# Kernel tuning notes

Measured on AMD Instinct MI355X. Metric: run time of the kernel, lower is better.

Reference implementation:

```python
import jax, jax.numpy as jnp
import numpy as np

HIDDEN = 2048
N_HEADS = 16
HEAD_DIM = 128
N_EXPERTS = 8
TOP_K = 2
INTER = 1024
EPS = 1e-5
ROPE_THETA = 10000.0
T = 2048


def rms_norm(x, w, eps=EPS):
    xf = x.astype(jnp.float32)
    return (xf * jax.lax.rsqrt(jnp.mean(xf * xf, axis=-1, keepdims=True) + eps)).astype(x.dtype) * w


def apply_rope(x, positions):
    # x: [T, H, D], NeoX-style half rotation
    d = x.shape[-1]
    inv_freq = 1.0 / (ROPE_THETA ** (jnp.arange(0, d, 2, dtype=jnp.float32) / d))
    ang = positions.astype(jnp.float32)[:, None] * inv_freq  # [T, D/2]
    cos = jnp.cos(ang)[:, None, :]
    sin = jnp.sin(ang)[:, None, :]
    x1, x2 = jnp.split(x, 2, axis=-1)
    return jnp.concatenate([x1 * cos - x2 * sin, x2 * cos + x1 * sin], axis=-1)


def setup_inputs() -> dict:
    key = jax.random.key(0)
    ks = jax.random.split(key, 8)
    s = 0.02
    return {
        "positions": jnp.arange(T, dtype=jnp.int32),
        "hidden_states": jax.random.normal(ks[0], (T, HIDDEN), jnp.float32),
        "qkv_w": jax.random.normal(ks[1], (3 * HIDDEN, HIDDEN), jnp.float32) * s,
        "o_w": jax.random.normal(ks[2], (HIDDEN, HIDDEN), jnp.float32) * s,
        "q_norm_w": jnp.ones((N_HEADS * HEAD_DIM,), jnp.float32),
        "k_norm_w": jnp.ones((N_HEADS * HEAD_DIM,), jnp.float32),
        "post_attn_norm_w": jnp.ones((HIDDEN,), jnp.float32),
        "post_ffn_norm_w": jnp.ones((HIDDEN,), jnp.float32),
        "gate_w": jax.random.normal(ks[3], (N_EXPERTS, HIDDEN), jnp.float32) * s,
        "w_gate": jax.random.normal(ks[4], (N_EXPERTS, INTER, HIDDEN), jnp.float32) * s,
        "w_up": jax.random.normal(ks[5], (N_EXPERTS, INTER, HIDDEN), jnp.float32) * s,
        "w_down": jax.random.normal(ks[6], (N_EXPERTS, HIDDEN, INTER), jnp.float32) * s,
    }


def attention(positions, x, qkv_w, o_w, q_norm_w, k_norm_w):
    qkv = x @ qkv_w.T  # [T, 3*HIDDEN]
    q, k, v = jnp.split(qkv, 3, axis=-1)
    q = rms_norm(q, q_norm_w)  # norm over full flat q dim (FlexOlmo/OLMoE style)
    k = rms_norm(k, k_norm_w)
    q = apply_rope(q.reshape(T, N_HEADS, HEAD_DIM), positions)
    k = apply_rope(k.reshape(T, N_HEADS, HEAD_DIM), positions)
    v = v.reshape(T, N_HEADS, HEAD_DIM)
    scale = 1.0 / np.sqrt(HEAD_DIM)
    scores = jnp.einsum('thd,shd->hts', q, k) * scale
    mask = jnp.tril(jnp.ones((T, T), bool))
    scores = jnp.where(mask[None], scores, -jnp.inf)
    p = jax.nn.softmax(scores, axis=-1)
    out = jnp.einsum('hts,shd->thd', p, v).reshape(T, HIDDEN)
    return out @ o_w.T


def moe(x, gate_w, w_gate, w_up, w_down):
    logits = (x @ gate_w.T).astype(jnp.float32)  # router_logits.float()
    probs = jax.nn.softmax(logits, axis=-1)
    topv, topi = jax.lax.top_k(probs, TOP_K)  # renormalize=False -> use raw softmax weights
    # dense per-expert combine weights: [T, E]
    wdense = jnp.zeros((T, N_EXPERTS), jnp.float32)
    wdense = jnp.sum(jax.nn.one_hot(topi, N_EXPERTS, dtype=jnp.float32) * topv[..., None], axis=1)
    # detach().clone() before dispatch (inference semantics: value unchanged)
    xe = jax.lax.stop_gradient(x)
    g = jnp.einsum('td,efd->tef', xe, w_gate)
    u = jnp.einsum('td,efd->tef', xe, w_up)
    h = jax.nn.silu(g) * u
    y = jnp.einsum('tef,edf->ted', h, w_down)
    return jnp.einsum('ted,te->td', y, wdense)


def reference(positions, hidden_states, qkv_w, o_w, q_norm_w, k_norm_w,
              post_attn_norm_w, post_ffn_norm_w, gate_w, w_gate, w_up, w_down):
    residual = hidden_states
    h = attention(positions, hidden_states, qkv_w, o_w, q_norm_w, k_norm_w)
    h = rms_norm(h, post_attn_norm_w)
    h = h + residual
    residual = h
    h = moe(h, gate_w, w_gate, w_up, w_down)
    h = rms_norm(h, post_ffn_norm_w)
    return residual + h
```

## Files before the change

kernel.cpp:

```cpp
#include <hip/hip_runtime.h>
#include <hip/hip_bf16.h>
#include <cmath>

#define TT 2048
#define HID 2048
#define NHEADS 16
#define HDIM 128
#define NEXP 8
#define INTERD 1024
#define EPSV 1e-5f

typedef short bf16x8 __attribute__((ext_vector_type(8)));
typedef float f32x4 __attribute__((ext_vector_type(4)));

__device__ __forceinline__ unsigned short f2bf(float f) {
    unsigned int u = __builtin_bit_cast(unsigned int, f);
    unsigned int r = (u + 0x7FFFu + ((u >> 16) & 1u)) >> 16;
    return (unsigned short)r;
}
__device__ __forceinline__ float bf2f(unsigned short h) {
    return __builtin_bit_cast(float, (unsigned int)h << 16);
}

__device__ __forceinline__ void gll16(const void* g, void* l) {
    __builtin_amdgcn_global_load_lds((const __attribute__((address_space(1))) void*)g,
                                     (__attribute__((address_space(3))) void*)l, 16, 0, 0);
}

__device__ __forceinline__ float block_reduce_sum_256(float v, float* red) {
    const int tid = threadIdx.x;
    red[tid] = v;
    __syncthreads();
    for (int s = 128; s > 0; s >>= 1) {
        if (tid < s) red[tid] += red[tid + s];
        __syncthreads();
    }
    float r = red[0];
    __syncthreads();
    return r;
}

__global__ __launch_bounds__(256) void split_f32k(const float* __restrict__ x,
                                                  unsigned short* __restrict__ hi,
                                                  unsigned short* __restrict__ lo, int n4) {
    int i = blockIdx.x * 256 + threadIdx.x;
    if (i >= n4) return;
    float4 v = reinterpret_cast<const float4*>(x)[i];
    float xs[4] = {v.x, v.y, v.z, v.w};
    unsigned short hs[4], ls[4];
#pragma unroll
    for (int u = 0; u < 4; ++u) {
        hs[u] = f2bf(xs[u]);
        ls[u] = f2bf(xs[u] - bf2f(hs[u]));
    }
    uint2 hp; hp.x = hs[0] | ((unsigned)hs[1] << 16); hp.y = hs[2] | ((unsigned)hs[3] << 16);
    uint2 lp; lp.x = ls[0] | ((unsigned)ls[1] << 16); lp.y = ls[2] | ((unsigned)ls[3] << 16);
    *reinterpret_cast<uint2*>(hi + (size_t)i * 4) = hp;
    *reinterpret_cast<uint2*>(lo + (size_t)i * 4) = lp;
}

#define GSTAGE(BUF, K0)                                                             \
    {                                                                               \
        char* base_ = (char*)Smem + (BUF) * 32768;                                  \
        _Pragma("unroll")                                                           \
        for (int i_ = 0; i_ < 2; ++i_) {                                            \
            int c_ = tid + i_ * 256;                                                \
            int r_ = c_ >> 2, s_ = c_ & 3;                                          \
            int ko_ = (K0) + (((s_ ^ ((r_ >> 1) & 3)) & 3) << 3);                   \
            gll16(Ah + (size_t)(m0 + r_) * lda + ko_, base_ + c_ * 16);             \
            gll16(Al + (size_t)(m0 + r_) * lda + ko_, base_ + 8192 + c_ * 16);      \
            gll16(Bh + (size_t)(n0 + r_) * K + ko_, base_ + 16384 + c_ * 16);       \
            gll16(Bl + (size_t)(n0 + r_) * K + ko_, base_ + 24576 + c_ * 16);       \
        }                                                                           \
    }

__global__ __launch_bounds__(256) void gemm_sp(const unsigned short* __restrict__ Ah,
                                               const unsigned short* __restrict__ Al,
                                               const unsigned short* __restrict__ Bh,
                                               const unsigned short* __restrict__ Bl,
                                               float* __restrict__ C, int N, int K, int lda) {
    const int nbx = gridDim.x;
    const int nwg = nbx * gridDim.y;
    const int orig = blockIdx.y * nbx + blockIdx.x;
    const int qq = nwg >> 3, rr = nwg & 7;
    const int xcd = orig & 7, loc = orig >> 3;
    const int wgid = (xcd < rr ? xcd * (qq + 1) : rr * (qq + 1) + (xcd - rr) * qq) + loc;
    const int m0 = (wgid / nbx) * 128, n0 = (wgid % nbx) * 128;

    __shared__ __align__(16) unsigned short Smem[2 * 4 * 128 * 32];
    const int tid = threadIdx.x;
    const int w = tid >> 6, l = tid & 63;
    const int lr = l & 15, lg = l >> 4;
    const int wm = w >> 1, wn = w & 1;

    f32x4 acc[4][4];
#pragma unroll
    for (int i = 0; i < 4; ++i)
#pragma unroll
        for (int j = 0; j < 4; ++j) acc[i][j] = f32x4{0.f, 0.f, 0.f, 0.f};

    const int nks = K >> 5;
    GSTAGE(0, 0);
    int cur = 0;
    for (int ks = 0; ks < nks; ++ks) {
        if (ks + 1 < nks) {
            GSTAGE(cur ^ 1, (ks + 1) << 5);
            asm volatile("s_waitcnt vmcnt(8)" ::: "memory");
        } else {
            asm volatile("s_waitcnt vmcnt(0)" ::: "memory");
        }
        __builtin_amdgcn_s_barrier();
        __builtin_amdgcn_sched_barrier(0);
        char* bb = (char*)Smem + cur * 32768;
        bf16x8 bhf[4], blf[4];
#pragma unroll
        for (int nt = 0; nt < 4; ++nt) {
            int row = wn * 64 + nt * 16 + lr;
            int off = row * 64 + (((lg ^ ((row >> 1) & 3)) & 3) << 4);
            bhf[nt] = *reinterpret_cast<const bf16x8*>(bb + 16384 + off);
            blf[nt] = *reinterpret_cast<const bf16x8*>(bb + 24576 + off);
        }
        __builtin_amdgcn_s_setprio(1);
#pragma unroll
        for (int mt = 0; mt < 4; ++mt) {
            int row = wm * 64 + mt * 16 + lr;
            int off = row * 64 + (((lg ^ ((row >> 1) & 3)) & 3) << 4);
            bf16x8 ahf = *reinterpret_cast<const bf16x8*>(bb + off);
            bf16x8 alf = *reinterpret_cast<const bf16x8*>(bb + 8192 + off);
#pragma unroll
            for (int nt = 0; nt < 4; ++nt) {
                acc[mt][nt] = __builtin_amdgcn_mfma_f32_16x16x32_bf16(ahf, bhf[nt], acc[mt][nt], 0, 0, 0);
                acc[mt][nt] = __builtin_amdgcn_mfma_f32_16x16x32_bf16(ahf, blf[nt], acc[mt][nt], 0, 0, 0);
                acc[mt][nt] = __builtin_amdgcn_mfma_f32_16x16x32_bf16(alf, bhf[nt], acc[mt][nt], 0, 0, 0);
            }
        }
        __builtin_amdgcn_s_setprio(0);
        asm volatile("s_waitcnt lgkmcnt(0)" ::: "memory");
        __builtin_amdgcn_s_barrier();
        __builtin_amdgcn_sched_barrier(0);
        cur ^= 1;
    }
#pragma unroll
    for (int mt = 0; mt < 4; ++mt) {
#pragma unroll
        for (int r = 0; r < 4; ++r) {
            size_t crow = (size_t)(m0 + wm * 64 + mt * 16 + lg * 4 + r) * N;
#pragma unroll
            for (int nt = 0; nt < 4; ++nt)
                C[crow + n0 + wn * 64 + nt * 16 + lr] = acc[mt][nt][r];
        }
    }
}

template<int ABF, int MODE>
__global__ __launch_bounds__(256) void gemm_moe(const void* __restrict__ Ap,
                                                const float* __restrict__ B,
                                                void* __restrict__ Cout,
                                                const float* __restrict__ gsrc,
                                                int N, int K, int lda,
                                                size_t strideB,
                                                const int* __restrict__ gather,
                                                const int* __restrict__ offs,
                                                const int* __restrict__ counts) {
    const int e = blockIdx.z;
    const int cnt = counts[e];
    const int base = offs[e];
    const int m0 = blockIdx.y * 64;
    if (m0 >= cnt) return;
    const int n0 = blockIdx.x * 128;
    const float* Bp = B + (size_t)e * strideB;

    __shared__ unsigned short smA[64 * 64];
    __shared__ unsigned short smB[128 * 64];
    __shared__ int rowsA[64];
    const int tid = threadIdx.x;
    if (tid < 64) {
        int rr = min(m0 + tid, cnt - 1);
        rowsA[tid] = gather ? gather[base + rr] : (base + rr);
    }
    __syncthreads();

    const int w = tid >> 6, l = tid & 63;
    const int lr = l & 15, lg = l >> 4;
    const int wm = w >> 1, wn = w & 1;
    char* sA = (char*)smA;
    char* sB = (char*)smB;

    f32x4 acc[2][4];
#pragma unroll
    for (int i = 0; i < 2; ++i)
#pragma unroll
        for (int j = 0; j < 4; ++j) acc[i][j] = f32x4{0.f, 0.f, 0.f, 0.f};

    for (int k0 = 0; k0 < K; k0 += 64) {
        if (ABF) {
            const unsigned short* Abf = (const unsigned short*)Ap;
#pragma unroll
            for (int i = 0; i < 2; ++i) {
                int slot = tid + i * 256;
                int r = slot >> 3, sg = slot & 7;
                uint4 v = *reinterpret_cast<const uint4*>(&Abf[(size_t)rowsA[r] * lda + k0 + sg * 8]);
                *reinterpret_cast<uint4*>(sA + r * 128 + ((sg * 16) ^ ((r & 7) << 4))) = v;
            }
        } else {
            const float* Af = (const float*)Ap;
#pragma unroll
            for (int i = 0; i < 4; ++i) {
                int slot = tid + i * 256;
                int r = slot >> 4, kq = slot & 15;
                float4 av = *reinterpret_cast<const float4*>(&Af[(size_t)rowsA[r] * lda + k0 + kq * 4]);
                uint2 pk;
                pk.x = (unsigned)f2bf(av.x) | ((unsigned)f2bf(av.y) << 16);
                pk.y = (unsigned)f2bf(av.z) | ((unsigned)f2bf(av.w) << 16);
                *reinterpret_cast<uint2*>(sA + r * 128 + ((kq * 8) ^ ((r & 7) << 4))) = pk;
            }
        }
#pragma unroll
        for (int i = 0; i < 8; ++i) {
            int slot = tid + i * 256;
            int r = slot >> 4, kq = slot & 15;
            float4 bv = *reinterpret_cast<const float4*>(&Bp[(size_t)(n0 + r) * K + k0 + kq * 4]);
            uint2 pk;
            pk.x = (unsigned)f2bf(bv.x) | ((unsigned)f2bf(bv.y) << 16);
            pk.y = (unsigned)f2bf(bv.z) | ((unsigned)f2bf(bv.w) << 16);
            *reinterpret_cast<uint2*>(sB + r * 128 + ((kq * 8) ^ ((r & 7) << 4))) = pk;
        }
        __syncthreads();
#pragma unroll
        for (int kk = 0; kk < 2; ++kk) {
            bf16x8 af[2], bfr[4];
#pragma unroll
            for (int mt = 0; mt < 2; ++mt) {
                int row = wm * 32 + mt * 16 + lr;
                af[mt] = *reinterpret_cast<const bf16x8*>(sA + row * 128 + ((kk * 64 + lg * 16) ^ ((row & 7) << 4)));
            }
#pragma unroll
            for (int nt = 0; nt < 4; ++nt) {
                int row = wn * 64 + nt * 16 + lr;
                bfr[nt] = *reinterpret_cast<const bf16x8*>(sB + row * 128 + ((kk * 64 + lg * 16) ^ ((row & 7) << 4)));
            }
            __builtin_amdgcn_s_setprio(1);
#pragma unroll
            for (int mt = 0; mt < 2; ++mt)
#pragma unroll
                for (int nt = 0; nt < 4; ++nt)
                    acc[mt][nt] = __builtin_amdgcn_mfma_f32_16x16x32_bf16(af[mt], bfr[nt], acc[mt][nt], 0, 0, 0);
            __builtin_amdgcn_s_setprio(0);
        }
        __syncthreads();
    }
#pragma unroll
    for (int mt = 0; mt < 2; ++mt) {
#pragma unroll
        for (int r = 0; r < 4; ++r) {
            int rowl = wm * 32 + mt * 16 + lg * 4 + r;
            if (m0 + rowl < cnt) {
                size_t crow = (size_t)(base + m0 + rowl) * N;
#pragma unroll
                for (int nt = 0; nt < 4; ++nt) {
                    size_t idx = crow + n0 + wn * 64 + nt * 16 + lr;
                    if (MODE == 1) {
                        float g = gsrc[idx];
                        ((unsigned short*)Cout)[idx] = f2bf(g / (1.f + expf(-g)) * acc[mt][nt][r]);
                    } else {
                        ((float*)Cout)[idx] = acc[mt][nt][r];
                    }
                }
            }
        }
    }
}

__global__ __launch_bounds__(256) void qknorm_rope_split(float* __restrict__ qkv,
                                                         const float* __restrict__ qw,
                                                         const float* __restrict__ kw,
                                                         const int* __restrict__ pos) {
    __shared__ float xbuf[2048];
    __shared__ float red[256];
    const int t = blockIdx.x, tid = threadIdx.x;
    unsigned short* row16 = (unsigned short*)(qkv + (size_t)t * 6144);
    const float pf = (float)pos[t];
    float vreg[8];
    const float* vsrc = qkv + (size_t)t * 6144 + 4096;
#pragma unroll
    for (int i = 0; i < 8; ++i) vreg[i] = vsrc[tid + i * 256];
    __syncthreads();
#pragma unroll
    for (int i = 0; i < 8; ++i) {
        int d = tid + i * 256;
        unsigned short hi = f2bf(vreg[i]);
        row16[8192 + d] = hi;
        row16[10240 + d] = f2bf(vreg[i] - bf2f(hi));
    }
    for (int part = 0; part < 2; ++part) {
        const float* x = qkv + (size_t)t * 6144 + part * 2048;
        const float* wn = part ? kw : qw;
        const int sbase = part ? 4096 : 0;
        const float outscale = part ? 1.0f : 0.08838834764831845f;
        float s = 0.f;
#pragma unroll
        for (int i = 0; i < 8; ++i) {
            int d = tid + i * 256;
            float v = x[d];
            xbuf[d] = v;
            s = fmaf(v, v, s);
        }
        float tot = block_reduce_sum_256(s, red);
        float scale = rsqrtf(tot * (1.f / HID) + EPSV);
#pragma unroll
        for (int p = tid; p < 1024; p += 256) {
            int hh = p >> 6, j = p & 63;
            int i1 = hh * 128 + j, i2 = i1 + 64;
            float x1 = xbuf[i1] * scale * wn[i1];
            float x2 = xbuf[i2] * scale * wn[i2];
            float invf = expf(-(float)j * 0.14391156831212787f);
            float ang = pf * invf;
            float sn, cs;
            sincosf(ang, &sn, &cs);
            float o1 = (x1 * cs - x2 * sn) * outscale;
            float o2 = (x2 * cs + x1 * sn) * outscale;
            unsigned short h1_ = f2bf(o1);
            row16[sbase + i1] = h1_;
            row16[sbase + 2048 + i1] = f2bf(o1 - bf2f(h1_));
            unsigned short h2_ = f2bf(o2);
            row16[sbase + i2] = h2_;
            row16[sbase + 2048 + i2] = f2bf(o2 - bf2f(h2_));
        }
        __syncthreads();
    }
}

__global__ __launch_bounds__(256) void kvprep(const unsigned short* __restrict__ qkv16,
                                              unsigned short* __restrict__ kt,
                                              unsigned short* __restrict__ vt) {
    const int C = blockIdx.x;
    const int h = blockIdx.y;
    const int tid = threadIdx.x;
#pragma unroll
    for (int p = 0; p < 2; ++p) {
#pragma unroll
        for (int i = 0; i < 4; ++i) {
            int slot = tid + i * 256;
            int r = slot >> 4, sg = slot & 15;
            uint4 v = *reinterpret_cast<const uint4*>(
                qkv16 + (size_t)(C * 64 + r) * 12288 + 4096 + p * 2048 + h * 128 + (sg ^ (r & 7)) * 8);
            *reinterpret_cast<uint4*>(kt + (size_t)(h * 32 + C) * 16384 + p * 8192 + slot * 8) = v;
        }
    }
    __shared__ unsigned short tile[64 * 128];
    char* tb = (char*)tile;
    for (int p = 0; p < 2; ++p) {
#pragma unroll
        for (int i = 0; i < 4; ++i) {
            int c = tid + i * 256;
            int r = c >> 4, dseg = c & 15;
            uint4 v = *reinterpret_cast<const uint4*>(
                qkv16 + (size_t)(C * 64 + r) * 12288 + 8192 + p * 2048 + h * 128 + dseg * 8);
            int swz = dseg ^ (r & 7) ^ (r >> 3);
            *reinterpret_cast<uint4*>(tb + r * 256 + swz * 16) = v;
        }
        __syncthreads();
        unsigned short* ob = vt + (size_t)(h * 32 + C) * 16384 + p * 8192;
#pragma unroll
        for (int i = 0; i < 4; ++i) {
            int c = tid + i * 256;
            int d = c >> 3, j = c & 7;
            unsigned short tmp[8];
#pragma unroll
            for (int u = 0; u < 8; ++u) {
                int s = 8 * j + u;
                int swz = (d >> 3) ^ (s & 7) ^ (s >> 3);
                tmp[u] = *reinterpret_cast<const unsigned short*>(tb + s * 256 + swz * 16 + (d & 7) * 2);
            }
            *reinterpret_cast<uint4*>(ob + (size_t)d * 64 + ((j ^ (d & 7)) * 8)) =
                *reinterpret_cast<const uint4*>(tmp);
        }
        __syncthreads();
    }
}

#define STAGE1(CIDX)                                                                   \
    {                                                                                  \
        const unsigned short* kb_ = kt + (size_t)(h * 32 + (CIDX)) * 16384;            \
        const unsigned short* vb_ = vt + (size_t)(h * 32 + (CIDX)) * 16384;            \
        _Pragma("unroll")                                                              \
        for (int p_ = 0; p_ < 2; ++p_) {                                               \
            _Pragma("unroll")                                                          \
            for (int i_ = 0; i_ < 4; ++i_) {                                           \
                int slot_ = tid + i_ * 256;                                            \
                gll16(kb_ + p_ * 8192 + slot_ * 8, kvb + p_ * 16384 + slot_ * 16);     \
                gll16(vb_ + p_ * 8192 + slot_ * 8, kvb + 32768 + p_ * 16384 + slot_ * 16); \
            }                                                                          \
        }                                                                              \
    }

__global__ __launch_bounds__(256) void attn_mfma(const unsigned short* __restrict__ qkv16,
                                                 const unsigned short* __restrict__ kt,
                                                 const unsigned short* __restrict__ vt,
                                                 unsigned short* __restrict__ oh,
                                                 unsigned short* __restrict__ ol) {
    const int g = blockIdx.x;
    const int rank = (g < 256) ? g : 767 - g;
    const int h = rank & 15;
    const int t0 = (31 - (rank >> 4)) * 64;
    const int tid = threadIdx.x;
    const int w = tid >> 6, l = tid & 63;
    const int lr = l & 15, lg = l >> 4;
    const size_t RS = 12288;
    __shared__ __align__(16) unsigned short KVs[32768];
    __shared__ unsigned short Ps[4][2 * 16 * 64];
    char* kvb = (char*)KVs;
    char* PsB = (char*)(Ps[w]);

    bf16x8 qh[4], ql[4];
    {
        const unsigned short* qp = qkv16 + (size_t)(t0 + w * 16 + lr) * RS + h * 128 + lg * 8;
#pragma unroll
        for (int kk = 0; kk < 4; ++kk) {
            qh[kk] = *reinterpret_cast<const bf16x8*>(qp + kk * 32);
            ql[kk] = *reinterpret_cast<const bf16x8*>(qp + 2048 + kk * 32);
        }
    }
    f32x4 oacc[8];
#pragma unroll
    for (int dt = 0; dt < 8; ++dt) oacc[dt] = f32x4{0.f, 0.f, 0.f, 0.f};
    float mrun[4] = {-INFINITY, -INFINITY, -INFINITY, -INFINITY};
    float lrun[4] = {0.f, 0.f, 0.f, 0.f};

    for (int s0 = 0; s0 <= t0; s0 += 64) {
        STAGE1(s0 >> 6);
        __syncthreads();
        char* KsB = kvb;
        char* VtB = kvb + 32768;

        f32x4 sc[4];
#pragma unroll
        for (int nt = 0; nt < 4; ++nt) sc[nt] = f32x4{0.f, 0.f, 0.f, 0.f};
        __builtin_amdgcn_s_setprio(1);
#pragma unroll
        for (int kk = 0; kk < 4; ++kk) {
#pragma unroll
            for (int nt = 0; nt < 4; ++nt) {
                int row = nt * 16 + lr;
                int off = row * 256 + ((kk * 64 + lg * 16) ^ ((row & 7) << 4));
                bf16x8 kh = *reinterpret_cast<const bf16x8*>(KsB + off);
                bf16x8 kl = *reinterpret_cast<const bf16x8*>(KsB + 16384 + off);
                sc[nt] = __builtin_amdgcn_mfma_f32_16x16x32_bf16(qh[kk], kh, sc[nt], 0, 0, 0);
                sc[nt] = __builtin_amdgcn_mfma_f32_16x16x32_bf16(ql[kk], kh, sc[nt], 0, 0, 0);
                sc[nt] = __builtin_amdgcn_mfma_f32_16x16x32_bf16(qh[kk], kl, sc[nt], 0, 0, 0);
            }
        }
        __builtin_amdgcn_s_setprio(0);
        float mnew[4], alpha[4], psum[4];
#pragma unroll
        for (int r = 0; r < 4; ++r) {
            int row_t = t0 + w * 16 + lg * 4 + r;
            float mx = mrun[r];
#pragma unroll
            for (int nt = 0; nt < 4; ++nt) {
                int col = s0 + nt * 16 + lr;
                float v = sc[nt][r];
                if (col > row_t) v = -INFINITY;
                sc[nt][r] = v;
                mx = fmaxf(mx, v);
            }
#pragma unroll
            for (int o = 1; o < 16; o <<= 1) mx = fmaxf(mx, __shfl_xor(mx, o));
            mnew[r] = mx;
            alpha[r] = expf(mrun[r] - mx);
            mrun[r] = mx;
            psum[r] = 0.f;
        }
#pragma unroll
        for (int nt = 0; nt < 4; ++nt) {
#pragma unroll
            for (int r = 0; r < 4; ++r) {
                float p = expf(sc[nt][r] - mnew[r]);
                psum[r] += p;
                int prow = lg * 4 + r;
                int off = prow * 128 + (((nt * 16 + lr) * 2) ^ ((prow & 7) << 4));
                unsigned short ph = f2bf(p);
                *reinterpret_cast<unsigned short*>(PsB + off) = ph;
                *reinterpret_cast<unsigned short*>(PsB + 2048 + off) = f2bf(p - bf2f(ph));
            }
        }
#pragma unroll
        for (int r = 0; r < 4; ++r) {
            float s = psum[r];
#pragma unroll
            for (int o = 1; o < 16; o <<= 1) s += __shfl_xor(s, o);
            lrun[r] = lrun[r] * alpha[r] + s;
        }
#pragma unroll
        for (int dt = 0; dt < 8; ++dt)
#pragma unroll
            for (int r = 0; r < 4; ++r) oacc[dt][r] *= alpha[r];
        bf16x8 ph[2], pl[2];
#pragma unroll
        for (int kk = 0; kk < 2; ++kk) {
            int off = lr * 128 + ((kk * 64 + lg * 16) ^ ((lr & 7) << 4));
            ph[kk] = *reinterpret_cast<const bf16x8*>(PsB + off);
            pl[kk] = *reinterpret_cast<const bf16x8*>(PsB + 2048 + off);
        }
        __builtin_amdgcn_s_setprio(1);
#pragma unroll
        for (int dt = 0; dt < 8; ++dt) {
            int row = dt * 16 + lr;
#pragma unroll
            for (int kk = 0; kk < 2; ++kk) {
                int off = row * 128 + ((kk * 64 + lg * 16) ^ ((row & 7) << 4));
                bf16x8 vh = *reinterpret_cast<const bf16x8*>(VtB + off);
                bf16x8 vl = *reinterpret_cast<const bf16x8*>(VtB + 16384 + off);
                oacc[dt] = __builtin_amdgcn_mfma_f32_16x16x32_bf16(ph[kk], vh, oacc[dt], 0, 0, 0);
                oacc[dt] = __builtin_amdgcn_mfma_f32_16x16x32_bf16(ph[kk], vl, oacc[dt], 0, 0, 0);
                oacc[dt] = __builtin_amdgcn_mfma_f32_16x16x32_bf16(pl[kk], vh, oacc[dt], 0, 0, 0);
            }
        }
        __builtin_amdgcn_s_setprio(0);
        __syncthreads();
    }
#pragma unroll
    for (int r = 0; r < 4; ++r) {
        float inv = 1.f / lrun[r];
        int row_t = t0 + w * 16 + lg * 4 + r;
#pragma unroll
        for (int dt = 0; dt < 8; ++dt) {
            float o = oacc[dt][r] * inv;
            unsigned short hb = f2bf(o);
            size_t idx = (size_t)row_t * 2048 + h * 128 + dt * 16 + lr;
            oh[idx] = hb;
            ol[idx] = f2bf(o - bf2f(hb));
        }
    }
}

__global__ __launch_bounds__(256) void add_rmsnorm(const float* __restrict__ resid,
                                                   const float* __restrict__ x,
                                                   const float* __restrict__ w,
                                                   float* __restrict__ out,
                                                   unsigned short* __restrict__ outbf) {
    __shared__ float red[256];
    const int t = blockIdx.x, tid = threadIdx.x;
    const float* xr = x + (size_t)t * HID;
    float v[8];
    float s = 0.f;
#pragma unroll
    for (int i = 0; i < 8; ++i) { v[i] = xr[tid + i * 256]; s = fmaf(v[i], v[i], s); }
    float tot = block_reduce_sum_256(s, red);
    float scale = rsqrtf(tot * (1.f / HID) + EPSV);
#pragma unroll
    for (int i = 0; i < 8; ++i) {
        int d = tid + i * 256;
        float o = resid[(size_t)t * HID + d] + v[i] * scale * w[d];
        out[(size_t)t * HID + d] = o;
        outbf[(size_t)t * HID + d] = f2bf(o);
    }
}

__global__ __launch_bounds__(64) void router_kernel(const float* __restrict__ h1,
                                                    const float* __restrict__ gate_w,
                                                    int* __restrict__ topi, float* __restrict__ topv,
                                                    int* __restrict__ slot_tk, int* __restrict__ counts) {
    const int t = blockIdx.x, lane = threadIdx.x;
    float acc[NEXP] = {};
    const float* x = h1 + (size_t)t * HID;
    for (int d = lane; d < HID; d += 64) {
        float xv = x[d];
#pragma unroll
        for (int e = 0; e < NEXP; ++e) acc[e] = fmaf(xv, gate_w[e * HID + d], acc[e]);
    }
#pragma unroll
    for (int e = 0; e < NEXP; ++e)
#pragma unroll
        for (int off = 32; off > 0; off >>= 1) acc[e] += __shfl_down(acc[e], off);
    if (lane == 0) {
        float mx = acc[0];
        for (int e = 1; e < NEXP; ++e) mx = fmaxf(mx, acc[e]);
        float p[NEXP], se = 0.f;
        for (int e = 0; e < NEXP; ++e) { p[e] = expf(acc[e] - mx); se += p[e]; }
        float inv = 1.f / se;
        for (int e = 0; e < NEXP; ++e) p[e] *= inv;
        int e1 = 0;
        for (int e = 1; e < NEXP; ++e) if (p[e] > p[e1]) e1 = e;
        int e2 = (e1 == 0) ? 1 : 0;
        for (int e = 0; e < NEXP; ++e) if (e != e1 && p[e] > p[e2]) e2 = e;
        topi[t * 2] = e1;     topv[t * 2] = p[e1];
        topi[t * 2 + 1] = e2; topv[t * 2 + 1] = p[e2];
        slot_tk[t * 2]     = atomicAdd(&counts[e1], 1);
        slot_tk[t * 2 + 1] = atomicAdd(&counts[e2], 1);
    }
}

__global__ void scan_kernel(const int* __restrict__ counts, int* __restrict__ offs) {
    int o = 0;
    for (int e = 0; e < NEXP; ++e) { offs[e] = o; o += counts[e]; }
}

__global__ __launch_bounds__(256) void map_kernel(const int* __restrict__ topi,
                                                  const int* __restrict__ slot_tk,
                                                  const int* __restrict__ offs,
                                                  int* __restrict__ token_of_row,
                                                  int* __restrict__ row_of_tk) {
    int idx = blockIdx.x * 256 + threadIdx.x;
    if (idx >= TT * 2) return;
    int e = topi[idx];
    int row = offs[e] + slot_tk[idx];
    token_of_row[row] = idx >> 1;
    row_of_tk[idx] = row;
}

__global__ __launch_bounds__(256) void final_combine(const float* __restrict__ h1,
                                                     const float* __restrict__ ypart,
                                                     const float* __restrict__ topv,
                                                     const int* __restrict__ row_of_tk,
                                                     const float* __restrict__ wffn,
                                                     float* __restrict__ out) {
    __shared__ float red[256];
    const int t = blockIdx.x, tid = threadIdx.x;
    const int r0 = row_of_tk[t * 2], r1 = row_of_tk[t * 2 + 1];
    const float w0 = topv[t * 2], w1 = topv[t * 2 + 1];
    const float* y0 = ypart + (size_t)r0 * HID;
    const float* y1 = ypart + (size_t)r1 * HID;
    float v[8];
    float s = 0.f;
#pragma unroll
    for (int i = 0; i < 8; ++i) {
        int d = tid + i * 256;
        v[i] = w0 * y0[d] + w1 * y1[d];
        s = fmaf(v[i], v[i], s);
    }
    float tot = block_reduce_sum_256(s, red);
    float scale = rsqrtf(tot * (1.f / HID) + EPSV);
#pragma unroll
    for (int i = 0; i < 8; ++i) {
        int d = tid + i * 256;
        out[(size_t)t * HID + d] = h1[(size_t)t * HID + d] + v[i] * scale * wffn[d];
    }
}

extern "C" void kernel_launch(void* const* d_in, const int* in_sizes, int n_in,
                              void* d_out, int out_size, void* d_ws, size_t ws_size,
                              hipStream_t stream) {
    const int*   positions = (const int*)d_in[0];
    const float* hidden    = (const float*)d_in[1];
    const float* qkv_w     = (const float*)d_in[2];
    const float* o_w       = (const float*)d_in[3];
    const float* q_norm_w  = (const float*)d_in[4];
    const float* k_norm_w  = (const float*)d_in[5];
    const float* post_attn = (const float*)d_in[6];
    const float* post_ffn  = (const float*)d_in[7];
    const float* gate_w    = (const float*)d_in[8];
    const float* w_gate    = (const float*)d_in[9];
    const float* w_up      = (const float*)d_in[10];
    const float* w_down    = (const float*)d_in[11];
    float* out = (float*)d_out;

    char* ws = (char*)d_ws;
    size_t off = 0;
    auto alloc = [&](size_t bytes) -> void* {
        void* p = ws + off;
        off += (bytes + 255) & ~(size_t)255;
        return p;
    };
    float*          qkvbuf = (float*)alloc((size_t)TT * 6144 * 4);
    unsigned short* hidsp  = (unsigned short*)alloc((size_t)TT * HID * 2 * 2);
    unsigned short* wsp    = (unsigned short*)alloc(((size_t)6144 * HID * 2 + (size_t)HID * HID * 2) * 2);
    float*          h1     = (float*)alloc((size_t)TT * HID * 4);
    unsigned short* h1bf   = (unsigned short*)alloc((size_t)TT * HID * 2);
    int*   topi   = (int*)alloc(TT * 2 * 4);
    float* topv   = (float*)alloc(TT * 2 * 4);
    int*   slot   = (int*)alloc(TT * 2 * 4);
    int*   rowtk  = (int*)alloc(TT * 2 * 4);
    int*   tokrow = (int*)alloc(TT * 2 * 4);
    int*   counts = (int*)alloc(8 * 4);
    int*   offsb  = (int*)alloc(8 * 4);
    if (off > ws_size) return;

    unsigned short* hid_hi   = hidsp;
    unsigned short* hid_lo   = hidsp + (size_t)TT * HID;
    unsigned short* attnO_hi = hid_hi;
    unsigned short* attnO_lo = hid_lo;
    unsigned short* qkvw_hi = wsp;
    unsigned short* qkvw_lo = wsp + (size_t)6144 * HID;
    unsigned short* ow_hi   = wsp + (size_t)2 * 6144 * HID;
    unsigned short* ow_lo   = ow_hi + (size_t)HID * HID;
    unsigned short* vtbuf   = wsp;
    unsigned short* ktbuf   = wsp + (size_t)TT * HID * 2;
    unsigned short* hinter = (unsigned short*)qkvbuf;
    float*          gbuf   = qkvbuf + (size_t)4096 * INTERD;
    float*          oOut   = qkvbuf + (size_t)8192 * INTERD;
    float*          ypart  = oOut;

    hipMemsetAsync(counts, 0, 8 * sizeof(int), stream);

    dim3 b256(256);
    split_f32k<<<dim3(TT * HID / 4 / 256), b256, 0, stream>>>(hidden, hid_hi, hid_lo, TT * HID / 4);
    split_f32k<<<dim3(6144 * HID / 4 / 256), b256, 0, stream>>>(qkv_w, qkvw_hi, qkvw_lo, 6144 * HID / 4);
    split_f32k<<<dim3(HID * HID / 4 / 256), b256, 0, stream>>>(o_w, ow_hi, ow_lo, HID * HID / 4);
    gemm_sp<<<dim3(6144 / 128, TT / 128), b256, 0, stream>>>(hid_hi, hid_lo, qkvw_hi, qkvw_lo,
                                                             qkvbuf, 6144, HID, HID);
    qknorm_rope_split<<<dim3(TT), b256, 0, stream>>>(qkvbuf, q_norm_w, k_norm_w, positions);
    kvprep<<<dim3(32, NHEADS), b256, 0, stream>>>((const unsigned short*)qkvbuf, ktbuf, vtbuf);
    attn_mfma<<<dim3(512), b256, 0, stream>>>((const unsigned short*)qkvbuf, ktbuf, vtbuf,
                                              attnO_hi, attnO_lo);
    gemm_sp<<<dim3(HID / 128, TT / 128), b256, 0, stream>>>(attnO_hi, attnO_lo, ow_hi, ow_lo,
                                                            oOut, HID, HID, HID);
    add_rmsnorm<<<dim3(TT), b256, 0, stream>>>(hidden, oOut, post_attn, h1, h1bf);
    router_kernel<<<dim3(TT), dim3(64), 0, stream>>>(h1, gate_w, topi, topv, slot, counts);
    scan_kernel<<<1, 1, 0, stream>>>(counts, offsb);
    map_kernel<<<dim3((TT * 2 + 255) / 256), b256, 0, stream>>>(topi, slot, offsb, tokrow, rowtk);
    gemm_moe<1, 0><<<dim3(INTERD / 128, TT * 2 / 64, NEXP), b256, 0, stream>>>(
        h1bf, w_gate, gbuf, nullptr, INTERD, HID, HID, (size_t)INTERD * HID, tokrow, offsb, counts);
    gemm_moe<1, 1><<<dim3(INTERD / 128, TT * 2 / 64, NEXP), b256, 0, stream>>>(
        h1bf, w_up, hinter, gbuf, INTERD, HID, HID, (size_t)INTERD * HID, tokrow, offsb, counts);
    gemm_moe<1, 0><<<dim3(HID / 128, TT * 2 / 64, NEXP), b256, 0, stream>>>(
        hinter, w_down, ypart, nullptr, HID, INTERD, INTERD, (size_t)HID * INTERD, nullptr, offsb, counts);
    final_combine<<<dim3(TT), b256, 0, stream>>>(h1, ypart, topv, rowtk, post_ffn, out);
}
```

Measured before the change: 660.2 us.

## Merge split kernels, drop scan kernel, use LDS-direct A loads, store bf16 MoE output

Merges the three fp32-to-bf16 hi/lo split launches into one kernel and removes the single-thread scan kernel by having each consumer compute expert offsets inline from counts. The MoE GEMM now loads A tiles straight into LDS with global_load_lds, using per-thread row indices computed up front in place of a shared row table and an extra barrier. The down projection writes its partial outputs as bf16 rather than fp32, which halves that write and the final combine's read but adds rounding before the weighted sum. The goal is fewer launches and less memory traffic, at some precision cost.

```diff
diff --git a/kernel.cpp b/kernel.cpp
--- a/kernel.cpp
+++ b/kernel.cpp
@@ -40,11 +40,17 @@
     return r;
 }
 
-__global__ __launch_bounds__(256) void split_f32k(const float* __restrict__ x,
-                                                  unsigned short* __restrict__ hi,
-                                                  unsigned short* __restrict__ lo, int n4) {
-    int i = blockIdx.x * 256 + threadIdx.x;
-    if (i >= n4) return;
+__global__ __launch_bounds__(256) void split3(const float* __restrict__ xh, unsigned short* __restrict__ hh,
+                                              unsigned short* __restrict__ hl,
+                                              const float* __restrict__ xq, unsigned short* __restrict__ qh,
+                                              unsigned short* __restrict__ ql,
+                                              const float* __restrict__ xo, unsigned short* __restrict__ oh,
+                                              unsigned short* __restrict__ ol) {
+    int b = blockIdx.x;
+    const float* x; unsigned short* hi; unsigned short* lo; int i;
+    if (b < 4096)       { x = xh; hi = hh; lo = hl; i = b * 256 + threadIdx.x; }
+    else if (b < 16384) { x = xq; hi = qh; lo = ql; i = (b - 4096) * 256 + threadIdx.x; }
+    else                { x = xo; hi = oh; lo = ol; i = (b - 16384) * 256 + threadIdx.x; }
     float4 v = reinterpret_cast<const float4*>(x)[i];
     float xs[4] = {v.x, v.y, v.z, v.w};
     unsigned short hs[4], ls[4];
@@ -152,40 +158,48 @@
     }
 }
 
-template<int ABF, int MODE>
-__global__ __launch_bounds__(256) void gemm_moe(const void* __restrict__ Ap,
+template<int GATHER, int MODE>
+__global__ __launch_bounds__(256) void gemm_moe(const unsigned short* __restrict__ Abf,
                                                 const float* __restrict__ B,
                                                 void* __restrict__ Cout,
                                                 const float* __restrict__ gsrc,
                                                 int N, int K, int lda,
                                                 size_t strideB,
                                                 const int* __restrict__ gather,
-                                                const int* __restrict__ offs,
                                                 const int* __restrict__ counts) {
     const int e = blockIdx.z;
     const int cnt = counts[e];
-    const int base = offs[e];
+    int base = 0;
+#pragma unroll
+    for (int i = 0; i < NEXP; ++i) base += (i < e) ? counts[i] : 0;
     const int m0 = blockIdx.y * 64;
     if (m0 >= cnt) return;
     const int n0 = blockIdx.x * 128;
     const float* Bp = B + (size_t)e * strideB;
 
-    __shared__ unsigned short smA[64 * 64];
+    __shared__ __align__(16) unsigned short smA[64 * 64];
     __shared__ unsigned short smB[128 * 64];
-    __shared__ int rowsA[64];
     const int tid = threadIdx.x;
-    if (tid < 64) {
-        int rr = min(m0 + tid, cnt - 1);
-        rowsA[tid] = gather ? gather[base + rr] : (base + rr);
-    }
-    __syncthreads();
-
     const int w = tid >> 6, l = tid & 63;
     const int lr = l & 15, lg = l >> 4;
     const int wm = w >> 1, wn = w & 1;
     char* sA = (char*)smA;
     char* sB = (char*)smB;
 
+    const int c0 = tid, c1 = tid + 256;
+    const int ra0 = c0 >> 3, sa0 = c0 & 7;
+    const int ra1 = c1 >> 3, sa1 = c1 & 7;
+    const int ka0 = ((sa0 ^ (ra0 & 7)) & 7) << 3;
+    const int ka1 = ((sa1 ^ (ra1 & 7)) & 7) << 3;
+    size_t arow0, arow1;
+    if (GATHER) {
+        arow0 = (size_t)gather[base + min(m0 + ra0, cnt - 1)];
+        arow1 = (size_t)gather[base + min(m0 + ra1, cnt - 1)];
+    } else {
+        arow0 = (size_t)(base + min(m0 + ra0, cnt - 1));
+        arow1 = (size_t)(base + min(m0 + ra1, cnt - 1));
+    }
+
     f32x4 acc[2][4];
 #pragma unroll
     for (int i = 0; i < 2; ++i)
@@ -193,28 +207,8 @@
         for (int j = 0; j < 4; ++j) acc[i][j] = f32x4{0.f, 0.f, 0.f, 0.f};
 
     for (int k0 = 0; k0 < K; k0 += 64) {
-        if (ABF) {
-            const unsigned short* Abf = (const unsigned short*)Ap;
-#pragma unroll
-            for (int i = 0; i < 2; ++i) {
-                int slot = tid + i * 256;
-                int r = slot >> 3, sg = slot & 7;
-                uint4 v = *reinterpret_cast<const uint4*>(&Abf[(size_t)rowsA[r] * lda + k0 + sg * 8]);
-                *reinterpret_cast<uint4*>(sA + r * 128 + ((sg * 16) ^ ((r & 7) << 4))) = v;
-            }
-        } else {
-            const float* Af = (const float*)Ap;
-#pragma unroll
-            for (int i = 0; i < 4; ++i) {
-                int slot = tid + i * 256;
-                int r = slot >> 4, kq = slot & 15;
-                float4 av = *reinterpret_cast<const float4*>(&Af[(size_t)rowsA[r] * lda + k0 + kq * 4]);
-                uint2 pk;
-                pk.x = (unsigned)f2bf(av.x) | ((unsigned)f2bf(av.y) << 16);
-                pk.y = (unsigned)f2bf(av.z) | ((unsigned)f2bf(av.w) << 16);
-                *reinterpret_cast<uint2*>(sA + r * 128 + ((kq * 8) ^ ((r & 7) << 4))) = pk;
-            }
-        }
+        gll16(Abf + arow0 * lda + k0 + ka0, sA + c0 * 16);
+        gll16(Abf + arow1 * lda + k0 + ka1, sA + c1 * 16);
 #pragma unroll
         for (int i = 0; i < 8; ++i) {
             int slot = tid + i * 256;
@@ -262,6 +256,8 @@
                     if (MODE == 1) {
                         float g = gsrc[idx];
                         ((unsigned short*)Cout)[idx] = f2bf(g / (1.f + expf(-g)) * acc[mt][nt][r]);
+                    } else if (MODE == 2) {
+                        ((unsigned short*)Cout)[idx] = f2bf(acc[mt][nt][r]);
                     } else {
                         ((float*)Cout)[idx] = acc[mt][nt][r];
                     }
@@ -591,26 +587,24 @@
     }
 }
 
-__global__ void scan_kernel(const int* __restrict__ counts, int* __restrict__ offs) {
-    int o = 0;
-    for (int e = 0; e < NEXP; ++e) { offs[e] = o; o += counts[e]; }
-}
-
 __global__ __launch_bounds__(256) void map_kernel(const int* __restrict__ topi,
                                                   const int* __restrict__ slot_tk,
-                                                  const int* __restrict__ offs,
+                                                  const int* __restrict__ counts,
                                                   int* __restrict__ token_of_row,
                                                   int* __restrict__ row_of_tk) {
     int idx = blockIdx.x * 256 + threadIdx.x;
     if (idx >= TT * 2) return;
     int e = topi[idx];
-    int row = offs[e] + slot_tk[idx];
+    int base = 0;
+#pragma unroll
+    for (int i = 0; i < NEXP; ++i) base += (i < e) ? counts[i] : 0;
+    int row = base + slot_tk[idx];
     token_of_row[row] = idx >> 1;
     row_of_tk[idx] = row;
 }
 
 __global__ __launch_bounds__(256) void final_combine(const float* __restrict__ h1,
-                                                     const float* __restrict__ ypart,
+                                                     const unsigned short* __restrict__ ypart,
                                                      const float* __restrict__ topv,
                                                      const int* __restrict__ row_of_tk,
                                                      const float* __restrict__ wffn,
@@ -619,14 +613,14 @@
     const int t = blockIdx.x, tid = threadIdx.x;
     const int r0 = row_of_tk[t * 2], r1 = row_of_tk[t * 2 + 1];
     const float w0 = topv[t * 2], w1 = topv[t * 2 + 1];
-    const float* y0 = ypart + (size_t)r0 * HID;
-    const float* y1 = ypart + (size_t)r1 * HID;
+    const unsigned short* y0 = ypart + (size_t)r0 * HID;
+    const unsigned short* y1 = ypart + (size_t)r1 * HID;
     float v[8];
     float s = 0.f;
 #pragma unroll
     for (int i = 0; i < 8; ++i) {
         int d = tid + i * 256;
-        v[i] = w0 * y0[d] + w1 * y1[d];
+        v[i] = w0 * bf2f(y0[d]) + w1 * bf2f(y1[d]);
         s = fmaf(v[i], v[i], s);
     }
     float tot = block_reduce_sum_256(s, red);
@@ -673,7 +667,6 @@
     int*   rowtk  = (int*)alloc(TT * 2 * 4);
     int*   tokrow = (int*)alloc(TT * 2 * 4);
     int*   counts = (int*)alloc(8 * 4);
-    int*   offsb  = (int*)alloc(8 * 4);
     if (off > ws_size) return;
 
     unsigned short* hid_hi   = hidsp;
@@ -689,14 +682,14 @@
     unsigned short* hinter = (unsigned short*)qkvbuf;
     float*          gbuf   = qkvbuf + (size_t)4096 * INTERD;
     float*          oOut   = qkvbuf + (size_t)8192 * INTERD;
-    float*          ypart  = oOut;
+    unsigned short* ypart  = (unsigned short*)oOut;
 
     hipMemsetAsync(counts, 0, 8 * sizeof(int), stream);
 
     dim3 b256(256);
-    split_f32k<<<dim3(TT * HID / 4 / 256), b256, 0, stream>>>(hidden, hid_hi, hid_lo, TT * HID / 4);
-    split_f32k<<<dim3(6144 * HID / 4 / 256), b256, 0, stream>>>(qkv_w, qkvw_hi, qkvw_lo, 6144 * HID / 4);
-    split_f32k<<<dim3(HID * HID / 4 / 256), b256, 0, stream>>>(o_w, ow_hi, ow_lo, HID * HID / 4);
+    split3<<<dim3(20480), b256, 0, stream>>>(hidden, hid_hi, hid_lo,
+                                             qkv_w, qkvw_hi, qkvw_lo,
+                                             o_w, ow_hi, ow_lo);
     gemm_sp<<<dim3(6144 / 128, TT / 128), b256, 0, stream>>>(hid_hi, hid_lo, qkvw_hi, qkvw_lo,
                                                              qkvbuf, 6144, HID, HID);
     qknorm_rope_split<<<dim3(TT), b256, 0, stream>>>(qkvbuf, q_norm_w, k_norm_w, positions);
@@ -707,13 +700,12 @@
                                                             oOut, HID, HID, HID);
     add_rmsnorm<<<dim3(TT), b256, 0, stream>>>(hidden, oOut, post_attn, h1, h1bf);
     router_kernel<<<dim3(TT), dim3(64), 0, stream>>>(h1, gate_w, topi, topv, slot, counts);
-    scan_kernel<<<1, 1, 0, stream>>>(counts, offsb);
-    map_kernel<<<dim3((TT * 2 + 255) / 256), b256, 0, stream>>>(topi, slot, offsb, tokrow, rowtk);
+    map_kernel<<<dim3((TT * 2 + 255) / 256), b256, 0, stream>>>(topi, slot, counts, tokrow, rowtk);
     gemm_moe<1, 0><<<dim3(INTERD / 128, TT * 2 / 64, NEXP), b256, 0, stream>>>(
-        h1bf, w_gate, gbuf, nullptr, INTERD, HID, HID, (size_t)INTERD * HID, tokrow, offsb, counts);
+        h1bf, w_gate, gbuf, nullptr, INTERD, HID, HID, (size_t)INTERD * HID, tokrow, counts);
     gemm_moe<1, 1><<<dim3(INTERD / 128, TT * 2 / 64, NEXP), b256, 0, stream>>>(
-        h1bf, w_up, hinter, gbuf, INTERD, HID, HID, (size_t)INTERD * HID, tokrow, offsb, counts);
-    gemm_moe<1, 0><<<dim3(HID / 128, TT * 2 / 64, NEXP), b256, 0, stream>>>(
-        hinter, w_down, ypart, nullptr, HID, INTERD, INTERD, (size_t)HID * INTERD, nullptr, offsb, counts);
+        h1bf, w_up, hinter, gbuf, INTERD, HID, HID, (size_t)INTERD * HID, tokrow, counts);
+    gemm_moe<0, 2><<<dim3(HID / 128, TT * 2 / 64, NEXP), b256, 0, stream>>>(
+        hinter, w_down, ypart, nullptr, HID, INTERD, INTERD, (size_t)HID * INTERD, nullptr, counts);
     final_combine<<<dim3(TT), b256, 0, stream>>>(h1, ypart, topv, rowtk, post_ffn, out);
 }
```

After: 662.3 us. About the same (+0.3%).
